# Optimization experiments

Measured on AMD Instinct MI355X. Metric: run time of the kernel, lower is better.

Reference implementation:

```python
import jax, jax.numpy as jnp
import numpy as np

GROUPS = 2
NUM_VARS = 320
VAR_DIM = 128  # vq_dim // groups = 256 // 2
CURR_TEMP = 2.0  # max_temp at num_updates=0
EPS = 1e-7


def setup_inputs() -> dict:
    key = jax.random.key(0)
    k1, k2, k3 = jax.random.split(key, 3)
    x = jax.random.normal(k1, (16, 2048, 768), dtype=jnp.float32)
    W = jax.random.normal(k2, (768, GROUPS * NUM_VARS), dtype=jnp.float32)  # std=1 per nn.init.normal_
    b = jnp.zeros((GROUPS * NUM_VARS,), dtype=jnp.float32)
    codebook = jax.random.uniform(k3, (1, GROUPS * NUM_VARS, VAR_DIM), dtype=jnp.float32)
    return {"x": x, "W": W, "b": b, "codebook": codebook}


def reference(x, W, b, codebook):
    # time_first=True -> x is [B, T, C]
    bsz, tsz, fsz = x.shape
    bt = bsz * tsz
    logits = x.reshape(bt, fsz) @ W + b                      # [BT, G*V]
    lg = logits.reshape(bt, GROUPS, NUM_VARS)                # [BT, G, V]

    # eval path: hard one-hot from argmax (self.training == False)
    k = jnp.argmax(lg, axis=-1)                              # [BT, G]
    hard = jax.nn.one_hot(k, NUM_VARS, dtype=logits.dtype)   # [BT, G, V]

    # codebook perplexity diagnostic
    avg_probs = jax.nn.softmax(lg.astype(jnp.float32), axis=-1).mean(axis=0)  # [G, V]
    ppl = jnp.exp(-jnp.sum(avg_probs * jnp.log(avg_probs + EPS), axis=-1)).sum()
    total_vars = GROUPS * NUM_VARS
    quantize_prob_ppl = (total_vars - ppl) / total_vars

    # one-hot x codebook multiply-sum == per-group gather, expressed as matmul
    cb = codebook.reshape(GROUPS, NUM_VARS, VAR_DIM)         # combine_groups=False
    q = jnp.einsum('ngv,gvd->ngd', hard, cb)                 # [BT, G, D]
    q = q.reshape(bsz, tsz, GROUPS * VAR_DIM)                # [B, T, vq_dim]
    return q, quantize_prob_ppl, jnp.float32(CURR_TEMP)
```

## Files before the change

kernel.cpp:

```cpp
#include <hip/hip_runtime.h>
#include <math.h>

#define GROUPS 2
#define NVARS  320
#define VDIM   128
#define NCOLS  640
#define FSZ    768
#define BTOT   32768
#define QDIM   256
#define KT     24
#define GAPTH  0.05f
#define LISTCAP 131072

typedef __bf16 bf16x8 __attribute__((ext_vector_type(8)));
typedef float  f32x4  __attribute__((ext_vector_type(4)));

__device__ __forceinline__ void gl_lds16(const void* g, void* l) {
    __builtin_amdgcn_global_load_lds(
        (const __attribute__((address_space(1))) unsigned int*)g,
        (__attribute__((address_space(3))) unsigned int*)l, 16, 0, 0);
}

__global__ __launch_bounds__(128) void xpre(
    const float* __restrict__ x, __bf16* __restrict__ xh, __bf16* __restrict__ xl, int row0)
{
    const int b = blockIdx.x;
    const int mblk = b / KT, kblk = b % KT;
    const int m = threadIdx.x;
    const float* src = x + (size_t)(row0 + mblk*128 + m) * FSZ + kblk*32;
    const size_t tbase = ((size_t)mblk*KT + kblk) * 4096;
    #pragma unroll
    for (int kq = 0; kq < 4; ++kq) {
        float4 a = ((const float4*)src)[kq*2];
        float4 c = ((const float4*)src)[kq*2+1];
        float vv[8] = {a.x,a.y,a.z,a.w,c.x,c.y,c.z,c.w};
        bf16x8 h, l;
        #pragma unroll
        for (int j = 0; j < 8; ++j) {
            __bf16 hh = (__bf16)vv[j];
            h[j] = hh;
            l[j] = (__bf16)(vv[j] - (float)hh);
        }
        ((bf16x8*)(xh + tbase))[kq*128 + m] = h;
        ((bf16x8*)(xl + tbase))[kq*128 + m] = l;
    }
}

__global__ __launch_bounds__(128) void wpre(
    const float* __restrict__ W, __bf16* __restrict__ wh, __bf16* __restrict__ wl)
{
    const int b = blockIdx.x;
    const int nblk = b / KT, kblk = b % KT;
    const int n = threadIdx.x;
    const size_t tbase = ((size_t)nblk*KT + kblk) * 4096;
    #pragma unroll
    for (int kq = 0; kq < 4; ++kq) {
        bf16x8 h, l;
        #pragma unroll
        for (int j = 0; j < 8; ++j) {
            float v = W[(size_t)(kblk*32 + kq*8 + j) * NCOLS + nblk*128 + n];
            __bf16 hh = (__bf16)v;
            h[j] = hh;
            l[j] = (__bf16)(v - (float)hh);
        }
        ((bf16x8*)(wh + tbase))[kq*128 + n] = h;
        ((bf16x8*)(wl + tbase))[kq*128 + n] = l;
    }
}

__global__ __launch_bounds__(256) void gemm_mfma(
    const __bf16* __restrict__ xh, const __bf16* __restrict__ xl,
    const __bf16* __restrict__ wh, const __bf16* __restrict__ wl,
    const float* __restrict__ bias, float* __restrict__ logits, int nwg)
{
    __shared__ __bf16 lds[16384];

    const int b = blockIdx.x;
    const int q8 = nwg >> 3, r8 = nwg & 7;
    const int xcd = b & 7, pos = b >> 3;
    const int L = (xcd < r8 ? xcd*(q8+1) : r8*(q8+1) + (xcd - r8)*q8) + pos;
    const int mblk = L / 5, nblk = L % 5;

    const int tid = threadIdx.x;
    const int w = tid >> 6, lane = tid & 63;
    const int wr = w >> 1, wc = w & 1;
    const int qq = lane >> 4, rr = lane & 15;

    f32x4 acc[4][4];
    #pragma unroll
    for (int i = 0; i < 4; ++i)
        #pragma unroll
        for (int j = 0; j < 4; ++j) acc[i][j] = (f32x4)0.f;

    const int ab = qq*128 + wr*64 + rr;
    const int bb = qq*128 + wc*64 + rr;

    for (int kt = 0; kt < KT; ++kt) {
        __syncthreads();
        const __bf16* ah_s = xh + ((size_t)mblk*KT + kt)*4096;
        const __bf16* al_s = xl + ((size_t)mblk*KT + kt)*4096;
        const __bf16* bh_s = wh + ((size_t)nblk*KT + kt)*4096;
        const __bf16* bl_s = wl + ((size_t)nblk*KT + kt)*4096;
        #pragma unroll
        for (int i = 0; i < 2; ++i) {
            const int u  = w*128 + i*64;
            const int el = (u + lane)*8;
            const int ed = u*8;
            gl_lds16(ah_s + el, &lds[0     + ed]);
            gl_lds16(al_s + el, &lds[4096  + ed]);
            gl_lds16(bh_s + el, &lds[8192  + ed]);
            gl_lds16(bl_s + el, &lds[12288 + ed]);
        }
        __syncthreads();

        const bf16x8* LAH = (const bf16x8*)&lds[0];
        const bf16x8* LAL = (const bf16x8*)&lds[4096];
        const bf16x8* LBH = (const bf16x8*)&lds[8192];
        const bf16x8* LBL = (const bf16x8*)&lds[12288];
        bf16x8 ah[4], al[4], bh[4], bl[4];
        #pragma unroll
        for (int mf = 0; mf < 4; ++mf) { ah[mf] = LAH[ab + mf*16]; al[mf] = LAL[ab + mf*16]; }
        #pragma unroll
        for (int nf = 0; nf < 4; ++nf) { bh[nf] = LBH[bb + nf*16]; bl[nf] = LBL[bb + nf*16]; }

        #pragma unroll
        for (int mf = 0; mf < 4; ++mf)
            #pragma unroll
            for (int nf = 0; nf < 4; ++nf) {
                acc[mf][nf] = __builtin_amdgcn_mfma_f32_16x16x32_bf16(ah[mf], bh[nf], acc[mf][nf], 0, 0, 0);
                acc[mf][nf] = __builtin_amdgcn_mfma_f32_16x16x32_bf16(al[mf], bh[nf], acc[mf][nf], 0, 0, 0);
                acc[mf][nf] = __builtin_amdgcn_mfma_f32_16x16x32_bf16(ah[mf], bl[nf], acc[mf][nf], 0, 0, 0);
            }
    }

    const int row0b = mblk*128 + wr*64;
    const int col0  = nblk*128 + wc*64;
    #pragma unroll
    for (int nf = 0; nf < 4; ++nf) {
        const int col = col0 + nf*16 + rr;
        const float bv = bias[col];
        #pragma unroll
        for (int mf = 0; mf < 4; ++mf) {
            const int rowb = row0b + mf*16 + qq*4;
            #pragma unroll
            for (int j = 0; j < 4; ++j)
                logits[(size_t)(rowb + j)*NCOLS + col] = acc[mf][nf][j] + bv;
        }
    }
}

#define RPB 16
__global__ __launch_bounds__(256) void rows_kernel(
    const float* __restrict__ logits, const float* __restrict__ cb,
    float* __restrict__ qout, float* __restrict__ partials,
    int* __restrict__ counter, int* __restrict__ list, int row0)
{
    __shared__ float probacc[4][NCOLS];
    const int tid = threadIdx.x, wid = tid >> 6, lane = tid & 63;
    for (int c = tid; c < 4*NCOLS; c += 256) ((float*)probacc)[c] = 0.f;
    __syncthreads();

    #pragma unroll
    for (int i = 0; i < RPB/4; ++i) {
        const int rl = blockIdx.x*RPB + wid*(RPB/4) + i;
        const float* lr = logits + (size_t)rl*NCOLS;
        const size_t grow = (size_t)row0 + rl;
        #pragma unroll
        for (int g = 0; g < GROUPS; ++g) {
            float v[5];
            #pragma unroll
            for (int j = 0; j < 5; ++j) v[j] = lr[g*NVARS + lane + 64*j];
            float m = v[0], m2 = -3.4e38f; int idx = lane;
            #pragma unroll
            for (int j = 1; j < 5; ++j) {
                if (v[j] > m) { m2 = m; m = v[j]; idx = lane + 64*j; }
                else m2 = fmaxf(m2, v[j]);
            }
            #pragma unroll
            for (int off = 32; off > 0; off >>= 1) {
                float om  = __shfl_xor(m, off);
                int   oi  = __shfl_xor(idx, off);
                float om2 = __shfl_xor(m2, off);
                if (om > m || (om == m && oi < idx)) { m2 = fmaxf(m, om2); m = om; idx = oi; }
                else m2 = fmaxf(m2, om);
            }
            float e[5], s = 0.f;
            #pragma unroll
            for (int j = 0; j < 5; ++j) { e[j] = __expf(v[j] - m); s += e[j]; }
            #pragma unroll
            for (int off = 32; off > 0; off >>= 1) s += __shfl_xor(s, off);
            const float inv = 1.0f / s;
            #pragma unroll
            for (int j = 0; j < 5; ++j)
                probacc[wid][g*NVARS + lane + 64*j] += e[j] * inv;
            if (lane == 0 && (m - m2) < GAPTH) {
                int p = atomicAdd(counter, 1);
                if (p < LISTCAP) list[p] = ((int)grow << 1) | g;
            }
            const float2* srcc = (const float2*)(cb + (size_t)(g*NVARS + idx)*VDIM);
            float2* dst = (float2*)(qout + grow*QDIM + (size_t)g*VDIM);
            dst[lane] = srcc[lane];
        }
    }
    __syncthreads();
    const size_t pb = (size_t)(row0 >> 4) + blockIdx.x;
    for (int c = tid; c < NCOLS; c += 256)
        partials[pb*NCOLS + c] = probacc[0][c] + probacc[1][c] + probacc[2][c] + probacc[3][c];
}

__global__ __launch_bounds__(256) void fixup_kernel(
    const float* __restrict__ x, const float* __restrict__ W,
    const float* __restrict__ bias, const float* __restrict__ cb,
    float* __restrict__ qout, const int* __restrict__ counter, const int* __restrict__ list)
{
    __shared__ float red[4][NVARS];
    int cnt = *counter; if (cnt > LISTCAP) cnt = LISTCAP;
    const int tid = threadIdx.x, w = tid >> 6, lane = tid & 63;

    for (int e = blockIdx.x; e < cnt; e += gridDim.x) {
        const int ent = list[e];
        const int row = ent >> 1, g = ent & 1;
        const float* xr = x + (size_t)row*FSZ;

        float acc[5] = {0.f, 0.f, 0.f, 0.f, 0.f};
        for (int k0 = w*192; k0 < w*192 + 192; k0 += 8) {
            const float4 xv0 = *(const float4*)(xr + k0);
            const float4 xv1 = *(const float4*)(xr + k0 + 4);
            const float xs[8] = {xv0.x, xv0.y, xv0.z, xv0.w, xv1.x, xv1.y, xv1.z, xv1.w};
            #pragma unroll
            for (int kk = 0; kk < 8; ++kk) {
                const float* wrow = W + (size_t)(k0 + kk)*NCOLS + g*NVARS;
                #pragma unroll
                for (int j = 0; j < 5; ++j)
                    acc[j] = fmaf(xs[kk], wrow[lane + 64*j], acc[j]);
            }
        }
        __syncthreads();
        #pragma unroll
        for (int j = 0; j < 5; ++j) red[w][lane + 64*j] = acc[j];
        __syncthreads();

        float v[5];
        #pragma unroll
        for (int j = 0; j < 5; ++j) {
            const int c = lane + 64*j;
            v[j] = red[0][c] + red[1][c] + red[2][c] + red[3][c] + bias[g*NVARS + c];
        }
        float m = v[0]; int idx = lane;
        #pragma unroll
        for (int j = 1; j < 5; ++j) if (v[j] > m) { m = v[j]; idx = lane + 64*j; }
        #pragma unroll
        for (int off = 32; off > 0; off >>= 1) {
            float om = __shfl_xor(m, off);
            int   oi = __shfl_xor(idx, off);
            if (om > m || (om == m && oi < idx)) { m = om; idx = oi; }
        }
        if (w == 0) {
            const float2* srcc = (const float2*)(cb + (size_t)(g*NVARS + idx)*VDIM);
            float2* dst = (float2*)(qout + (size_t)row*QDIM + (size_t)g*VDIM);
            dst[lane] = srcc[lane];
        }
    }
}

#define REDBLK 16
__global__ __launch_bounds__(256) void reduce_kernel(
    const float* __restrict__ partials, float* __restrict__ avg)
{
    const int tid = threadIdx.x;
    const int p0 = blockIdx.x * (BTOT/RPB/REDBLK);
    float s[3] = {0.f, 0.f, 0.f};
    for (int p = p0; p < p0 + BTOT/RPB/REDBLK; ++p) {
        const float* row = partials + (size_t)p*NCOLS;
        #pragma unroll
        for (int i = 0; i < 3; ++i) {
            const int c = tid + i*256;
            if (c < NCOLS) s[i] += row[c];
        }
    }
    #pragma unroll
    for (int i = 0; i < 3; ++i) {
        const int c = tid + i*256;
        if (c < NCOLS) atomicAdd(&avg[c], s[i]);
    }
}

__global__ __launch_bounds__(64) void finalize_kernel(
    const float* __restrict__ avg, float* __restrict__ out)
{
    const int lane = threadIdx.x;
    float pp[GROUPS];
    #pragma unroll
    for (int g = 0; g < GROUPS; ++g) {
        float s = 0.f;
        #pragma unroll
        for (int j = 0; j < 5; ++j) {
            float p = avg[g*NVARS + lane + 64*j] * (1.0f/(float)BTOT);
            s += p * logf(p + 1e-7f);
        }
        #pragma unroll
        for (int off = 32; off > 0; off >>= 1) s += __shfl_xor(s, off);
        pp[g] = expf(-s);
    }
    if (lane == 0) {
        float ppl = pp[0] + pp[1];
        out[(size_t)BTOT*QDIM]     = ((float)NCOLS - ppl) / (float)NCOLS;
        out[(size_t)BTOT*QDIM + 1] = 2.0f;
    }
}

extern "C" void kernel_launch(void* const* d_in, const int* in_sizes, int n_in,
                              void* d_out, int out_size, void* d_ws, size_t ws_size,
                              hipStream_t stream)
{
    const float* x  = (const float*)d_in[0];
    const float* W  = (const float*)d_in[1];
    const float* b  = (const float*)d_in[2];
    const float* cb = (const float*)d_in[3];
    float* out = (float*)d_out;

    char* ws = (char*)d_ws;
    int*   counter  = (int*)ws;
    float* avg      = (float*)(ws + 1024);
    int*   list     = (int*)(ws + 8192);
    float* partials = (float*)(ws + 532480);
    __bf16* wh      = (__bf16*)(ws + 5775360);
    __bf16* wl      = (__bf16*)(ws + 6758400);
    char* chunkbase = ws + 7741440;

    long long avail = (long long)ws_size - 7741440;
    long long rmax = avail / 5632;
    if (rmax > BTOT) rmax = BTOT;
    if (rmax < 128)  rmax = 128;
    int chunks = (int)((BTOT + rmax - 1) / rmax);
    int R = ((BTOT / chunks + 127) / 128) * 128;

    hipMemsetAsync(ws, 0, 4096, stream);
    wpre<<<5*KT, 128, 0, stream>>>(W, wh, wl);

    for (int row0 = 0; row0 < BTOT; row0 += R) {
        int Rc = BTOT - row0; if (Rc > R) Rc = R;
        const int nmb = Rc / 128;
        __bf16* xh = (__bf16*)chunkbase;
        __bf16* xl = xh + (size_t)nmb*KT*4096;
        float* logits = (float*)(xl + (size_t)nmb*KT*4096);

        xpre<<<nmb*KT, 128, 0, stream>>>(x, xh, xl, row0);
        const int nwg = nmb * 5;
        gemm_mfma<<<nwg, 256, 0, stream>>>(xh, xl, wh, wl, b, logits, nwg);
        rows_kernel<<<Rc/RPB, 256, 0, stream>>>(logits, cb, out, partials, counter, list, row0);
    }
    fixup_kernel<<<512, 256, 0, stream>>>(x, W, b, cb, out, counter, list);
    reduce_kernel<<<REDBLK, 256, 0, stream>>>(partials, avg);
    finalize_kernel<<<1, 64, 0, stream>>>(avg, out);
}
```

Before: 430.0 us.

## Fuse x bf16 hi/lo split into GEMM, drop xpre pre-pass kernel

Removes the separate xpre kernel that split x into bf16 high/low tiles in global memory. The GEMM now loads fp32 x directly, with the next k-tile's loads issued after the barrier as a register prefetch, then splits and writes the pieces into LDS itself. This avoids writing and re-reading the bf16 x buffers and lets larger row chunks fit in the workspace. In exchange each x tile is converted 5 times (once per N block), the kernel uses more registers, and an occupancy hint is added to the launch bounds.

```diff
diff --git a/kernel.cpp b/kernel.cpp
--- a/kernel.cpp
+++ b/kernel.cpp
@@ -13,37 +13,13 @@
 #define LISTCAP 131072
 
 typedef __bf16 bf16x8 __attribute__((ext_vector_type(8)));
+typedef __bf16 bf16x4 __attribute__((ext_vector_type(4)));
 typedef float  f32x4  __attribute__((ext_vector_type(4)));
 
 __device__ __forceinline__ void gl_lds16(const void* g, void* l) {
     __builtin_amdgcn_global_load_lds(
         (const __attribute__((address_space(1))) unsigned int*)g,
         (__attribute__((address_space(3))) unsigned int*)l, 16, 0, 0);
-}
-
-__global__ __launch_bounds__(128) void xpre(
-    const float* __restrict__ x, __bf16* __restrict__ xh, __bf16* __restrict__ xl, int row0)
-{
-    const int b = blockIdx.x;
-    const int mblk = b / KT, kblk = b % KT;
-    const int m = threadIdx.x;
-    const float* src = x + (size_t)(row0 + mblk*128 + m) * FSZ + kblk*32;
-    const size_t tbase = ((size_t)mblk*KT + kblk) * 4096;
-    #pragma unroll
-    for (int kq = 0; kq < 4; ++kq) {
-        float4 a = ((const float4*)src)[kq*2];
-        float4 c = ((const float4*)src)[kq*2+1];
-        float vv[8] = {a.x,a.y,a.z,a.w,c.x,c.y,c.z,c.w};
-        bf16x8 h, l;
-        #pragma unroll
-        for (int j = 0; j < 8; ++j) {
-            __bf16 hh = (__bf16)vv[j];
-            h[j] = hh;
-            l[j] = (__bf16)(vv[j] - (float)hh);
-        }
-        ((bf16x8*)(xh + tbase))[kq*128 + m] = h;
-        ((bf16x8*)(xl + tbase))[kq*128 + m] = l;
-    }
 }
 
 __global__ __launch_bounds__(128) void wpre(
@@ -68,10 +44,10 @@
     }
 }
 
-__global__ __launch_bounds__(256) void gemm_mfma(
-    const __bf16* __restrict__ xh, const __bf16* __restrict__ xl,
+__global__ __launch_bounds__(256, 4) void gemm_fused(
+    const float* __restrict__ x,
     const __bf16* __restrict__ wh, const __bf16* __restrict__ wl,
-    const float* __restrict__ bias, float* __restrict__ logits, int nwg)
+    const float* __restrict__ bias, float* __restrict__ logits, int nwg, int row0)
 {
     __shared__ __bf16 lds[16384];
 
@@ -95,23 +71,53 @@
     const int ab = qq*128 + wr*64 + rr;
     const int bb = qq*128 + wc*64 + rr;
 
+    const int prow = tid >> 3;
+    const int pc   = tid & 7;
+    const float* xbase = x + (size_t)(row0 + mblk*128 + prow) * FSZ + pc*4;
+    const int aelem = ((pc >> 1)*128)*8 + (pc & 1)*4 + prow*8;
+
+    float4 xv0 = *(const float4*)(xbase);
+    float4 xv1 = *(const float4*)(xbase + 32*FSZ);
+    float4 xv2 = *(const float4*)(xbase + 64*FSZ);
+    float4 xv3 = *(const float4*)(xbase + 96*FSZ);
+
     for (int kt = 0; kt < KT; ++kt) {
         __syncthreads();
-        const __bf16* ah_s = xh + ((size_t)mblk*KT + kt)*4096;
-        const __bf16* al_s = xl + ((size_t)mblk*KT + kt)*4096;
+        {
+            float4 xr[4] = {xv0, xv1, xv2, xv3};
+            #pragma unroll
+            for (int r = 0; r < 4; ++r) {
+                const float vv[4] = {xr[r].x, xr[r].y, xr[r].z, xr[r].w};
+                bf16x4 h, l;
+                #pragma unroll
+                for (int j = 0; j < 4; ++j) {
+                    __bf16 hh = (__bf16)vv[j];
+                    h[j] = hh;
+                    l[j] = (__bf16)(vv[j] - (float)hh);
+                }
+                const int e = aelem + r*256;
+                *(bf16x4*)&lds[e]        = h;
+                *(bf16x4*)&lds[4096 + e] = l;
+            }
+        }
         const __bf16* bh_s = wh + ((size_t)nblk*KT + kt)*4096;
         const __bf16* bl_s = wl + ((size_t)nblk*KT + kt)*4096;
         #pragma unroll
         for (int i = 0; i < 2; ++i) {
-            const int u  = w*128 + i*64;
-            const int el = (u + lane)*8;
-            const int ed = u*8;
-            gl_lds16(ah_s + el, &lds[0     + ed]);
-            gl_lds16(al_s + el, &lds[4096  + ed]);
-            gl_lds16(bh_s + el, &lds[8192  + ed]);
-            gl_lds16(bl_s + el, &lds[12288 + ed]);
+            const int u = w*128 + i*64;
+            gl_lds16(bh_s + (u + lane)*8, &lds[8192  + u*8]);
+            gl_lds16(bl_s + (u + lane)*8, &lds[12288 + u*8]);
         }
         __syncthreads();
+
+        {
+            const int ktn = (kt + 1 < KT) ? kt + 1 : kt;
+            const float* xp = xbase + ktn*32;
+            xv0 = *(const float4*)(xp);
+            xv1 = *(const float4*)(xp + 32*FSZ);
+            xv2 = *(const float4*)(xp + 64*FSZ);
+            xv3 = *(const float4*)(xp + 96*FSZ);
+        }
 
         const bf16x8* LAH = (const bf16x8*)&lds[0];
         const bf16x8* LAL = (const bf16x8*)&lds[4096];
@@ -224,9 +230,9 @@
 
         float acc[5] = {0.f, 0.f, 0.f, 0.f, 0.f};
         for (int k0 = w*192; k0 < w*192 + 192; k0 += 8) {
-            const float4 xv0 = *(const float4*)(xr + k0);
-            const float4 xv1 = *(const float4*)(xr + k0 + 4);
-            const float xs[8] = {xv0.x, xv0.y, xv0.z, xv0.w, xv1.x, xv1.y, xv1.z, xv1.w};
+            const float4 xva = *(const float4*)(xr + k0);
+            const float4 xvb = *(const float4*)(xr + k0 + 4);
+            const float xs[8] = {xva.x, xva.y, xva.z, xva.w, xvb.x, xvb.y, xvb.z, xvb.w};
             #pragma unroll
             for (int kk = 0; kk < 8; ++kk) {
                 const float* wrow = W + (size_t)(k0 + kk)*NCOLS + g*NVARS;
@@ -326,14 +332,13 @@
     float* partials = (float*)(ws + 532480);
     __bf16* wh      = (__bf16*)(ws + 5775360);
     __bf16* wl      = (__bf16*)(ws + 6758400);
-    char* chunkbase = ws + 7741440;
+    float* logits   = (float*)(ws + 7741440);
 
     long long avail = (long long)ws_size - 7741440;
-    long long rmax = avail / 5632;
+    long long rmax = avail / 2560;
     if (rmax > BTOT) rmax = BTOT;
-    if (rmax < 128)  rmax = 128;
-    int chunks = (int)((BTOT + rmax - 1) / rmax);
-    int R = ((BTOT / chunks + 127) / 128) * 128;
+    int R = (int)((rmax / 128) * 128);
+    if (R < 128) R = 128;
 
     hipMemsetAsync(ws, 0, 4096, stream);
     wpre<<<5*KT, 128, 0, stream>>>(W, wh, wl);
@@ -341,13 +346,8 @@
     for (int row0 = 0; row0 < BTOT; row0 += R) {
         int Rc = BTOT - row0; if (Rc > R) Rc = R;
         const int nmb = Rc / 128;
-        __bf16* xh = (__bf16*)chunkbase;
-        __bf16* xl = xh + (size_t)nmb*KT*4096;
-        float* logits = (float*)(xl + (size_t)nmb*KT*4096);
-
-        xpre<<<nmb*KT, 128, 0, stream>>>(x, xh, xl, row0);
         const int nwg = nmb * 5;
-        gemm_mfma<<<nwg, 256, 0, stream>>>(xh, xl, wh, wl, b, logits, nwg);
+        gemm_fused<<<nwg, 256, 0, stream>>>(x, wh, wl, b, logits, nwg, row0);
         rows_kernel<<<Rc/RPB, 256, 0, stream>>>(logits, cb, out, partials, counter, list, row0);
     }
     fixup_kernel<<<512, 256, 0, stream>>>(x, W, b, cb, out, counter, list);
```

Measured after the change: 391.2 us. 1.1x faster.
